# Performance work log

Measured on AMD Instinct MI355X. Metric: run time of the kernel, lower is better.

## Reference

```python
import jax, jax.numpy as jnp
import numpy as np

N, E, G = 100000, 1600000, 1000
F_IN, H, C = 16, 64, 2
EPS = 1e-5


def setup_inputs() -> dict:
    key = jax.random.key(0)
    ks = jax.random.split(key, 8)

    def lin(k, i, o):
        return (jax.random.normal(k, (i, o), jnp.float32) / np.float32(np.sqrt(i)))

    return {
        "x": jax.random.normal(ks[0], (N, F_IN), jnp.float32),
        "edge_index": jax.random.randint(ks[1], (2, E), 0, N),
        "batch": jnp.sort(jax.random.randint(ks[2], (N,), 0, G)),
        # GraphNorm params: weight=1, bias=0, mean_scale(alpha)=1 (PyG init)
        "gn0_w": jnp.ones(F_IN, jnp.float32), "gn0_b": jnp.zeros(F_IN, jnp.float32), "gn0_a": jnp.ones(F_IN, jnp.float32),
        "W1": lin(ks[3], F_IN, H), "b1": jnp.zeros(H, jnp.float32),
        "gn1_w": jnp.ones(H, jnp.float32), "gn1_b": jnp.zeros(H, jnp.float32), "gn1_a": jnp.ones(H, jnp.float32),
        "W2": lin(ks[4], H, H), "b2": jnp.zeros(H, jnp.float32),
        "gn2_w": jnp.ones(H, jnp.float32), "gn2_b": jnp.zeros(H, jnp.float32), "gn2_a": jnp.ones(H, jnp.float32),
        "W3": lin(ks[5], H, H), "b3": jnp.zeros(H, jnp.float32),
        "Wd": lin(ks[6], H, H), "bd": jnp.zeros(H, jnp.float32),
        "Wo": lin(ks[7], H, C), "bo": jnp.zeros(C, jnp.float32),
    }


def _graph_norm(x, batch, w, b, a):
    counts = jnp.maximum(jax.ops.segment_sum(jnp.ones(x.shape[0], x.dtype), batch, G), 1.0)[:, None]
    mean = jax.ops.segment_sum(x, batch, G) / counts          # [G, F]
    out = x - a * mean[batch]
    var = jax.ops.segment_sum(out * out, batch, G) / counts   # [G, F]
    return w * (out * jax.lax.rsqrt(var + EPS)[batch]) + b


def _gcn_conv(x, W, b, src, dst):
    # PyG GCNConv: D^{-1/2}(A+I)D^{-1/2} X W + b, deg includes self-loop
    h = x @ W                                                  # [N, out]
    deg = jax.ops.segment_sum(jnp.ones(src.shape[0], x.dtype), dst, N) + 1.0
    dinv = jax.lax.rsqrt(deg)
    msg = h[src] * (dinv[src] * dinv[dst])[:, None]            # [E, out]
    agg = jax.ops.segment_sum(msg, dst, N) + h / deg[:, None]  # self-loop term: 1/deg
    return agg + b


def reference(x, edge_index, batch, gn0_w, gn0_b, gn0_a, W1, b1,
              gn1_w, gn1_b, gn1_a, W2, b2, gn2_w, gn2_b, gn2_a,
              W3, b3, Wd, bd, Wo, bo):
    src, dst = edge_index[0], edge_index[1]
    x = _graph_norm(x, batch, gn0_w, gn0_b, gn0_a)
    x = jax.nn.relu(_gcn_conv(x, W1, b1, src, dst))
    x = _graph_norm(x, batch, gn1_w, gn1_b, gn1_a)
    x = jax.nn.relu(_gcn_conv(x, W2, b2, src, dst))
    x = _graph_norm(x, batch, gn2_w, gn2_b, gn2_a)
    x = jax.nn.relu(_gcn_conv(x, W3, b3, src, dst))
    counts = jnp.maximum(jax.ops.segment_sum(jnp.ones(N, x.dtype), batch, G), 1.0)
    pooled = jax.ops.segment_sum(x, batch, G) / counts[:, None]  # global_mean_pool [G, H]
    # dropout p=0.5 is identity in eval mode
    h = jax.nn.relu(pooled @ Wd + bd)
    logits = h @ Wo + bo
    return jax.nn.softmax(logits, axis=1)
```

## Files before the change

### kernel.cpp

```cpp
#include <hip/hip_runtime.h>
#include <hip/hip_fp16.h>
#include <math.h>

#define NB_NODES 100000
#define NB_EDGES 1600000
#define NB_GRAPHS 1000
#define CAP 232
#define NBLK1 400
#define CHUNK 4000
#define NBUCK 391
#define BCAP 4608
constexpr float GN_EPS = 1e-5f;

__global__ __launch_bounds__(256) void k1_hist(const int* __restrict__ dst,
    int* __restrict__ hist, const int* __restrict__ batch, int* __restrict__ gstart) {
    __shared__ int h[NBUCK];
    int tid = threadIdx.x;
    for (int i = tid; i < NBUCK; i += 256) h[i] = 0;
    if (blockIdx.x < 4) {
        int g = blockIdx.x * 256 + tid;
        if (g <= NB_GRAPHS) {
            int lo = 0, hi = NB_NODES;
            while (lo < hi) {
                int mid = (lo + hi) >> 1;
                if (batch[mid] < g) lo = mid + 1; else hi = mid;
            }
            gstart[g] = lo;
        }
    }
    __syncthreads();
    int base = blockIdx.x * CHUNK;
    for (int i = tid; i < CHUNK; i += 256) atomicAdd(&h[dst[base + i] >> 8], 1);
    __syncthreads();
    for (int i = tid; i < NBUCK; i += 256) hist[blockIdx.x * NBUCK + i] = h[i];
}

__global__ __launch_bounds__(512) void k2a_scan(int* __restrict__ hist,
                                                int* __restrict__ total) {
    __shared__ int s[512];
    int b = blockIdx.x;
    int tid = threadIdx.x;
    int v = (tid < NBLK1) ? hist[tid * NBUCK + b] : 0;
    s[tid] = v;
    __syncthreads();
    for (int o = 1; o < 512; o <<= 1) {
        int t = (tid >= o) ? s[tid - o] : 0;
        __syncthreads();
        s[tid] += t;
        __syncthreads();
    }
    if (tid < NBLK1) hist[tid * NBUCK + b] = s[tid] - v;
    if (tid == 511) total[b] = s[511];
}

__global__ __launch_bounds__(512) void k2b_scan(const int* __restrict__ total,
                                                int* __restrict__ base) {
    __shared__ int s[512];
    int tid = threadIdx.x;
    int v = (tid < NBUCK) ? total[tid] : 0;
    s[tid] = v;
    __syncthreads();
    for (int o = 1; o < 512; o <<= 1) {
        int t = (tid >= o) ? s[tid - o] : 0;
        __syncthreads();
        s[tid] += t;
        __syncthreads();
    }
    if (tid < NBUCK) base[tid] = s[tid] - v;
    if (tid == NBUCK) base[NBUCK] = NB_EDGES;
}

__global__ __launch_bounds__(256) void k3_scatter(const int* __restrict__ ei,
    const int* __restrict__ hist, const int* __restrict__ base,
    unsigned int* __restrict__ ebuf) {
    __shared__ int cur[NBUCK];
    int tid = threadIdx.x;
    for (int i = tid; i < NBUCK; i += 256)
        cur[i] = base[i] + hist[blockIdx.x * NBUCK + i];
    __syncthreads();
    int eb = blockIdx.x * CHUNK;
    for (int i = tid; i < CHUNK; i += 256) {
        int e = eb + i;
        int sidx = ei[e];
        int d = ei[NB_EDGES + e];
        int pos = atomicAdd(&cur[d >> 8], 1);
        ebuf[pos] = (unsigned int)sidx | ((unsigned int)(d & 255) << 24);
    }
}

__global__ __launch_bounds__(256) void k4_fine(const unsigned int* __restrict__ ebuf,
    const int* __restrict__ base, int* __restrict__ csr_src, int* __restrict__ rowptr,
    float* __restrict__ dinv) {
    __shared__ unsigned int epk[BCAP];
    __shared__ int outb[BCAP];
    __shared__ int cnt[256];
    __shared__ int sbuf[256];
    __shared__ int cur2[256];
    int b = blockIdx.x;
    int tid = threadIdx.x;
    int eb = base[b], ee = base[b + 1];
    int m = ee - eb;
    if (m > BCAP) m = BCAP;
    for (int i = tid; i < m; i += 256) epk[i] = ebuf[eb + i];
    cnt[tid] = 0;
    __syncthreads();
    for (int i = tid; i < m; i += 256) atomicAdd(&cnt[epk[i] >> 24], 1);
    __syncthreads();
    int c = cnt[tid];
    sbuf[tid] = c;
    __syncthreads();
    for (int o = 1; o < 256; o <<= 1) {
        int t = (tid >= o) ? sbuf[tid - o] : 0;
        __syncthreads();
        sbuf[tid] += t;
        __syncthreads();
    }
    int off = sbuf[tid] - c;
    cur2[tid] = off;
    __syncthreads();
    for (int i = tid; i < m; i += 256) {
        unsigned int p = epk[i];
        int r = atomicAdd(&cur2[p >> 24], 1);
        outb[r] = (int)(p & 0x00FFFFFFu);
    }
    __syncthreads();
    for (int i = tid; i < m; i += 256) csr_src[eb + i] = outb[i];
    int node = b * 256 + tid;
    if (node < NB_NODES) {
        rowptr[node] = eb + off;
        dinv[node] = rsqrtf((float)(c + 1));
    }
    if (b == 0 && tid == 0) rowptr[NB_NODES] = NB_EDGES;
}

union HU {
    uint4 u;
    __half2 h[4];
};

__device__ __forceinline__ void pkacc(__half2* a, uint4 v) {
    HU x; x.u = v;
    a[0] = __hadd2(a[0], x.h[0]);
    a[1] = __hadd2(a[1], x.h[1]);
    a[2] = __hadd2(a[2], x.h[2]);
    a[3] = __hadd2(a[3], x.h[3]);
}

__device__ __forceinline__ __half2 shxor_h2(__half2 v, int m) {
    union { __half2 h; int i; } u;
    u.h = v;
    u.i = __shfl_xor(u.i, m, 64);
    return u.h;
}

__global__ __launch_bounds__(256) void aggregate_h_k(const __half* __restrict__ hs,
    const int* __restrict__ rowptr, const int* __restrict__ csr_src,
    const float* __restrict__ dinv, const float* __restrict__ bias,
    __half* __restrict__ out) {
    const uint4* hsv = (const uint4*)hs;
    int wv = blockIdx.x * 4 + (threadIdx.x >> 6);
    int lane = threadIdx.x & 63;
    int f8 = lane & 7;
    int e8 = lane >> 3;
    int n0 = __builtin_amdgcn_readfirstlane(wv * 2);
    int n1 = n0 + 1;
    int s0 = rowptr[n0], e0 = rowptr[n0 + 1], e1 = rowptr[n1 + 1];
    int s1 = e0;
    int d0 = e0 - s0, d1 = e1 - s1;
    const uint4 Z = {0u, 0u, 0u, 0u};
    int idx0 = (lane < d0) ? csr_src[s0 + lane] : -1;
    int idx1 = (lane < d1) ? csr_src[s1 + lane] : -1;
    uint4 self0 = Z, self1 = Z;
    if (e8 == 0) self0 = hsv[(size_t)n0 * 8 + f8];
    if (e8 == 1) self1 = hsv[(size_t)n1 * 8 + f8];
    uint4 g0[4], g1[4];
#pragma unroll
    for (int b = 0; b < 4; b++) {
        int u = __shfl(idx0, b * 8 + e8, 64);
        g0[b] = Z;
        if (u >= 0) g0[b] = hsv[(size_t)u * 8 + f8];
        int v = __shfl(idx1, b * 8 + e8, 64);
        g1[b] = Z;
        if (v >= 0) g1[b] = hsv[(size_t)v * 8 + f8];
    }
    __half2 acc0[4], acc1[4];
    acc0[0] = acc0[1] = acc0[2] = acc0[3] = __half2{__half(0.f), __half(0.f)};
    acc1[0] = acc1[1] = acc1[2] = acc1[3] = __half2{__half(0.f), __half(0.f)};
    pkacc(acc0, self0);
    pkacc(acc1, self1);
#pragma unroll
    for (int b = 0; b < 4; b++) { pkacc(acc0, g0[b]); pkacc(acc1, g1[b]); }
    int tb0 = (d0 + 7) >> 3, tb1 = (d1 + 7) >> 3;
    for (int b = 4; b < tb0 && b < 8; b++) {
        int u = __shfl(idx0, b * 8 + e8, 64);
        if (u >= 0) pkacc(acc0, hsv[(size_t)u * 8 + f8]);
    }
    for (int b = 4; b < tb1 && b < 8; b++) {
        int v = __shfl(idx1, b * 8 + e8, 64);
        if (v >= 0) pkacc(acc1, hsv[(size_t)v * 8 + f8]);
    }
    for (int b = 8; b < tb0; b++) {
        int j = s0 + b * 8 + e8;
        if (j < e0) { int u = csr_src[j]; pkacc(acc0, hsv[(size_t)u * 8 + f8]); }
    }
    for (int b = 8; b < tb1; b++) {
        int j = s1 + b * 8 + e8;
        if (j < e1) { int v = csr_src[j]; pkacc(acc1, hsv[(size_t)v * 8 + f8]); }
    }
#pragma unroll
    for (int c = 0; c < 4; c++) {
        __half2 t = acc0[c];
        t = __hadd2(t, shxor_h2(t, 8));
        t = __hadd2(t, shxor_h2(t, 16));
        t = __hadd2(t, shxor_h2(t, 32));
        acc0[c] = t;
        __half2 u = acc1[c];
        u = __hadd2(u, shxor_h2(u, 8));
        u = __hadd2(u, shxor_h2(u, 16));
        u = __hadd2(u, shxor_h2(u, 32));
        acc1[c] = u;
    }
    if (e8 < 2) {
        int node = (e8 == 0) ? n0 : n1;
        const __half2* acc = (e8 == 0) ? acc0 : acc1;
        float dn = dinv[node];
        const float4* b4 = (const float4*)bias;
        float4 blo = b4[f8 * 2], bhi = b4[f8 * 2 + 1];
        float2 f0 = __half22float2(acc[0]);
        float2 f1 = __half22float2(acc[1]);
        float2 f2 = __half22float2(acc[2]);
        float2 f3 = __half22float2(acc[3]);
        float r[8];
        r[0] = fmaf(f0.x, dn, blo.x); r[1] = fmaf(f0.y, dn, blo.y);
        r[2] = fmaf(f1.x, dn, blo.z); r[3] = fmaf(f1.y, dn, blo.w);
        r[4] = fmaf(f2.x, dn, bhi.x); r[5] = fmaf(f2.y, dn, bhi.y);
        r[6] = fmaf(f3.x, dn, bhi.z); r[7] = fmaf(f3.y, dn, bhi.w);
#pragma unroll
        for (int c = 0; c < 8; c++) r[c] = r[c] > 0.f ? r[c] : 0.f;
        HU o;
        o.h[0] = __floats2half2_rn(r[0], r[1]);
        o.h[1] = __floats2half2_rn(r[2], r[3]);
        o.h[2] = __floats2half2_rn(r[4], r[5]);
        o.h[3] = __floats2half2_rn(r[6], r[7]);
        ((uint4*)out)[(size_t)node * 8 + f8] = o.u;
    }
}

__global__ __launch_bounds__(512) void normlin_k(const __half* __restrict__ A,
    const int* __restrict__ gstart, const float* __restrict__ gw,
    const float* __restrict__ gb, const float* __restrict__ ga,
    const float* __restrict__ W, const float* __restrict__ dinv,
    __half* __restrict__ out) {
    __shared__ float sW[64 * 64];
    __shared__ float red[512], red2[512];
    __shared__ float sam[64], ssc[64];
    __shared__ float srow[8 * 64];
    int tid = threadIdx.x, lane = tid & 63, wid = tid >> 6;
    int g = blockIdx.x;
    int s = gstart[g], e = gstart[g + 1], cnt = e - s;
    float cntf = (float)(cnt > 1 ? cnt : 1);
    for (int i = tid; i < 64 * 64; i += 512) sW[i] = W[i];
    float sum = 0.f, sq = 0.f;
    for (int i = s + wid; i < e; i += 8) {
        float v = __half2float(A[(size_t)i * 64 + lane]);
        sum += v;
        sq = fmaf(v, v, sq);
    }
    red[tid] = sum; red2[tid] = sq;
    __syncthreads();
    for (int st = 4; st > 0; st >>= 1) {
        if (wid < st) { red[tid] += red[tid + st * 64]; red2[tid] += red2[tid + st * 64]; }
        __syncthreads();
    }
    if (tid < 64) {
        float m = red[tid] / cntf, q = red2[tid] / cntf;
        float am = ga[tid] * m;
        float var = q - 2.f * am * m + am * am;
        sam[tid] = am;
        ssc[tid] = gw[tid] * rsqrtf(var + GN_EPS);
    }
    __syncthreads();
    float am = sam[lane], sc = ssc[lane], bb = gb[lane];
    for (int i = s + wid; i < e; i += 8) {
        float nv = (__half2float(A[(size_t)i * 64 + lane]) - am) * sc + bb;
        srow[wid * 64 + lane] = nv;
        float acc = 0.f;
#pragma unroll
        for (int k = 0; k < 64; k++) acc = fmaf(srow[wid * 64 + k], sW[k * 64 + lane], acc);
        out[(size_t)i * 64 + lane] = __float2half(acc * dinv[i]);
    }
}

__device__ __forceinline__ void l0_body(float* rows, int cnt, int s,
    const float* __restrict__ x, const float* __restrict__ gw,
    const float* __restrict__ gb, const float* __restrict__ ga,
    const float* sW, const float* __restrict__ dinv, __half* __restrict__ hs_out,
    float* red, float* red2, float* sstat, float* sscale, int tid) {
    int f = tid & 15, r = tid >> 4;
    int lane = tid & 63, wid = tid >> 6;
    float cntf = (float)(cnt > 1 ? cnt : 1);
    float sum = 0.f, sq = 0.f;
    for (int i = r; i < cnt; i += 32) {
        float v = x[(size_t)(s + i) * 16 + f];
        rows[i * 16 + f] = v;
        sum += v;
        sq = fmaf(v, v, sq);
    }
    red[tid] = sum; red2[tid] = sq;
    __syncthreads();
    for (int st = 16; st > 0; st >>= 1) {
        if (r < st) { red[tid] += red[tid + st * 16]; red2[tid] += red2[tid + st * 16]; }
        __syncthreads();
    }
    if (tid < 16) {
        float m = red[tid] / cntf, q = red2[tid] / cntf;
        float am = ga[tid] * m;
        sstat[tid] = am;
        sscale[tid] = gw[tid] * rsqrtf(q - 2.f * am * m + am * am + GN_EPS);
    }
    __syncthreads();
    float am = sstat[f], sc = sscale[f], bb = gb[f];
    for (int i = r; i < cnt; i += 32) rows[i * 16 + f] = (rows[i * 16 + f] - am) * sc + bb;
    __syncthreads();
    for (int i = wid; i < cnt; i += 8) {
        float acc = 0.f;
#pragma unroll
        for (int k = 0; k < 16; k++) acc = fmaf(rows[i * 16 + k], sW[k * 64 + lane], acc);
        hs_out[(size_t)(s + i) * 64 + lane] = __float2half(acc * dinv[s + i]);
    }
}

__global__ __launch_bounds__(512) void layer0_k(const float* __restrict__ x,
    const int* __restrict__ gstart, const float* __restrict__ gw,
    const float* __restrict__ gb, const float* __restrict__ ga,
    const float* __restrict__ W, const float* __restrict__ dinv,
    __half* __restrict__ hs_out, float* __restrict__ spill16) {
    __shared__ float sRows[CAP * 16];
    __shared__ float sW[16 * 64];
    __shared__ float red[512], red2[512];
    __shared__ float sstat[16], sscale[16];
    int tid = threadIdx.x;
    int g = blockIdx.x;
    int s = gstart[g], e = gstart[g + 1], cnt = e - s;
    for (int i = tid; i < 16 * 64; i += 512) sW[i] = W[i];
    __syncthreads();
    if (cnt <= CAP)
        l0_body(sRows, cnt, s, x, gw, gb, ga, sW, dinv, hs_out, red, red2, sstat, sscale, tid);
    else
        l0_body(spill16 + (size_t)s * 16, cnt, s, x, gw, gb, ga, sW, dinv, hs_out, red, red2, sstat, sscale, tid);
}

__global__ void pool_head_k(const __half* __restrict__ x, const int* __restrict__ gstart,
                            const float* __restrict__ Wd, const float* __restrict__ bd,
                            const float* __restrict__ Wo, const float* __restrict__ bo,
                            float* __restrict__ out) {
    __shared__ float red[256];
    __shared__ float sp[64];
    __shared__ float sh[64];
    __shared__ float sl[2];
    int g = blockIdx.x;
    int s = gstart[g], e = gstart[g + 1];
    int cnt = e - s;
    float cntf = (float)(cnt > 1 ? cnt : 1);
    int tid = threadIdx.x;
    int f = tid & 63, r = tid >> 6;
    float sum = 0.f;
    for (int i = s + r; i < e; i += 4) sum += __half2float(x[(size_t)i * 64 + f]);
    red[tid] = sum;
    __syncthreads();
    for (int st = 2; st > 0; st >>= 1) {
        if (r < st) red[tid] += red[tid + st * 64];
        __syncthreads();
    }
    if (tid < 64) sp[tid] = red[tid] / cntf;
    __syncthreads();
    if (tid < 64) {
        float acc = bd[tid];
        for (int k = 0; k < 64; k++) acc = fmaf(sp[k], Wd[k * 64 + tid], acc);
        sh[tid] = acc > 0.f ? acc : 0.f;
    }
    __syncthreads();
    if (tid < 2) {
        float l = bo[tid];
        for (int k = 0; k < 64; k++) l = fmaf(sh[k], Wo[k * 2 + tid], l);
        sl[tid] = l;
    }
    __syncthreads();
    if (tid < 2) {
        float m = fmaxf(sl[0], sl[1]);
        float e0 = expf(sl[0] - m), e1 = expf(sl[1] - m);
        out[g * 2 + tid] = (tid == 0 ? e0 : e1) / (e0 + e1);
    }
}

extern "C" void kernel_launch(void* const* d_in, const int* in_sizes, int n_in,
                              void* d_out, int out_size, void* d_ws, size_t ws_size,
                              hipStream_t stream) {
    const float* x    = (const float*)d_in[0];
    const int* ei     = (const int*)d_in[1];
    const int* batch  = (const int*)d_in[2];
    const float* gn0w = (const float*)d_in[3];
    const float* gn0b = (const float*)d_in[4];
    const float* gn0a = (const float*)d_in[5];
    const float* W1   = (const float*)d_in[6];
    const float* b1   = (const float*)d_in[7];
    const float* gn1w = (const float*)d_in[8];
    const float* gn1b = (const float*)d_in[9];
    const float* gn1a = (const float*)d_in[10];
    const float* W2   = (const float*)d_in[11];
    const float* b2   = (const float*)d_in[12];
    const float* gn2w = (const float*)d_in[13];
    const float* gn2b = (const float*)d_in[14];
    const float* gn2a = (const float*)d_in[15];
    const float* W3   = (const float*)d_in[16];
    const float* b3   = (const float*)d_in[17];
    const float* Wd   = (const float*)d_in[18];
    const float* bd   = (const float*)d_in[19];
    const float* Wo   = (const float*)d_in[20];
    const float* bo   = (const float*)d_in[21];

    char* p = (char*)d_ws;
    auto alloc = [&](size_t bytes) -> void* {
        void* r = (void*)p;
        p += (bytes + 255) & ~(size_t)255;
        return r;
    };
    __half* A        = (__half*)alloc((size_t)NB_NODES * 64 * 2);
    __half* B        = (__half*)alloc((size_t)NB_NODES * 64 * 2);
    int* rowptr      = (int*)alloc((size_t)(NB_NODES + 1) * 4);
    unsigned* ebuf   = (unsigned*)alloc((size_t)NB_EDGES * 4);
    int* csr_src     = (int*)alloc((size_t)NB_EDGES * 4);
    int* hist        = (int*)alloc((size_t)NBLK1 * NBUCK * 4);
    int* total       = (int*)alloc((size_t)NBUCK * 4);
    int* basearr     = (int*)alloc((size_t)(NBUCK + 1) * 4);
    float* dinv      = (float*)alloc((size_t)NB_NODES * 4);
    int* gstart      = (int*)alloc((size_t)(NB_GRAPHS + 1) * 4);
    float* spill16   = (float*)alloc((size_t)NB_NODES * 16 * 4);

    k1_hist<<<NBLK1, 256, 0, stream>>>(ei + NB_EDGES, hist, batch, gstart);
    k2a_scan<<<NBUCK, 512, 0, stream>>>(hist, total);
    k2b_scan<<<1, 512, 0, stream>>>(total, basearr);
    k3_scatter<<<NBLK1, 256, 0, stream>>>(ei, hist, basearr, ebuf);
    k4_fine<<<NBUCK, 256, 0, stream>>>(ebuf, basearr, csr_src, rowptr, dinv);

    layer0_k<<<NB_GRAPHS, 512, 0, stream>>>(x, gstart, gn0w, gn0b, gn0a, W1, dinv, B, spill16);
    aggregate_h_k<<<12500, 256, 0, stream>>>(B, rowptr, csr_src, dinv, b1, A);
    normlin_k<<<NB_GRAPHS, 512, 0, stream>>>(A, gstart, gn1w, gn1b, gn1a, W2, dinv, B);
    aggregate_h_k<<<12500, 256, 0, stream>>>(B, rowptr, csr_src, dinv, b2, A);
    normlin_k<<<NB_GRAPHS, 512, 0, stream>>>(A, gstart, gn2w, gn2b, gn2a, W3, dinv, B);
    aggregate_h_k<<<12500, 256, 0, stream>>>(B, rowptr, csr_src, dinv, b3, A);
    pool_head_k<<<NB_GRAPHS, 256, 0, stream>>>(A, gstart, Wd, bd, Wo, bo, (float*)d_out);
}
```

Before: 321.5 us.

## Fuse CSR-build kernels into one persistent kernel with grid barriers

Merges the five CSR-construction kernels (histogram, two scans, scatter, fine sort) into a single 400-block kernel separated by software grid barriers built on atomic counters, plus a memset to reset the counters. The aim is to remove the launch gaps between several small kernels. The change relies on all 400 blocks being resident at once, since otherwise the barrier deadlocks. It also adds spin-wait overhead and a larger static shared allocation per block.

```diff
diff --git a/kernel.cpp b/kernel.cpp
--- a/kernel.cpp
+++ b/kernel.cpp
@@ -12,125 +12,152 @@
 #define BCAP 4608
 constexpr float GN_EPS = 1e-5f;
 
-__global__ __launch_bounds__(256) void k1_hist(const int* __restrict__ dst,
-    int* __restrict__ hist, const int* __restrict__ batch, int* __restrict__ gstart) {
-    __shared__ int h[NBUCK];
+__device__ __forceinline__ void gbar(int* bar, int idx, int n) {
+    __syncthreads();
+    if (threadIdx.x == 0) {
+        __threadfence();
+        atomicAdd(&bar[idx], 1);
+        while (atomicAdd(&bar[idx], 0) < n) __builtin_amdgcn_s_sleep(8);
+        __threadfence();
+    }
+    __syncthreads();
+}
+
+__global__ __launch_bounds__(256) void csr_build_k(const int* __restrict__ ei,
+    const int* __restrict__ batch, int* __restrict__ gstart, int* __restrict__ hist,
+    int* __restrict__ total, int* __restrict__ base, unsigned int* __restrict__ ebuf,
+    int* __restrict__ csr_src, int* __restrict__ rowptr, float* __restrict__ dinv,
+    int* __restrict__ bar) {
+    __shared__ int shmem[2 * BCAP + 768];
+    const int* dst = ei + NB_EDGES;
     int tid = threadIdx.x;
-    for (int i = tid; i < NBUCK; i += 256) h[i] = 0;
-    if (blockIdx.x < 4) {
-        int g = blockIdx.x * 256 + tid;
-        if (g <= NB_GRAPHS) {
-            int lo = 0, hi = NB_NODES;
-            while (lo < hi) {
-                int mid = (lo + hi) >> 1;
-                if (batch[mid] < g) lo = mid + 1; else hi = mid;
+    int blk = blockIdx.x;
+
+    {
+        int* h = shmem;
+        for (int i = tid; i < NBUCK; i += 256) h[i] = 0;
+        if (blk < 4) {
+            int g = blk * 256 + tid;
+            if (g <= NB_GRAPHS) {
+                int lo = 0, hi = NB_NODES;
+                while (lo < hi) {
+                    int mid = (lo + hi) >> 1;
+                    if (batch[mid] < g) lo = mid + 1; else hi = mid;
+                }
+                gstart[g] = lo;
             }
-            gstart[g] = lo;
-        }
-    }
-    __syncthreads();
-    int base = blockIdx.x * CHUNK;
-    for (int i = tid; i < CHUNK; i += 256) atomicAdd(&h[dst[base + i] >> 8], 1);
-    __syncthreads();
-    for (int i = tid; i < NBUCK; i += 256) hist[blockIdx.x * NBUCK + i] = h[i];
-}
-
-__global__ __launch_bounds__(512) void k2a_scan(int* __restrict__ hist,
-                                                int* __restrict__ total) {
-    __shared__ int s[512];
-    int b = blockIdx.x;
-    int tid = threadIdx.x;
-    int v = (tid < NBLK1) ? hist[tid * NBUCK + b] : 0;
-    s[tid] = v;
-    __syncthreads();
-    for (int o = 1; o < 512; o <<= 1) {
-        int t = (tid >= o) ? s[tid - o] : 0;
-        __syncthreads();
-        s[tid] += t;
-        __syncthreads();
-    }
-    if (tid < NBLK1) hist[tid * NBUCK + b] = s[tid] - v;
-    if (tid == 511) total[b] = s[511];
-}
-
-__global__ __launch_bounds__(512) void k2b_scan(const int* __restrict__ total,
-                                                int* __restrict__ base) {
-    __shared__ int s[512];
-    int tid = threadIdx.x;
-    int v = (tid < NBUCK) ? total[tid] : 0;
-    s[tid] = v;
-    __syncthreads();
-    for (int o = 1; o < 512; o <<= 1) {
-        int t = (tid >= o) ? s[tid - o] : 0;
-        __syncthreads();
-        s[tid] += t;
-        __syncthreads();
-    }
-    if (tid < NBUCK) base[tid] = s[tid] - v;
-    if (tid == NBUCK) base[NBUCK] = NB_EDGES;
-}
-
-__global__ __launch_bounds__(256) void k3_scatter(const int* __restrict__ ei,
-    const int* __restrict__ hist, const int* __restrict__ base,
-    unsigned int* __restrict__ ebuf) {
-    __shared__ int cur[NBUCK];
-    int tid = threadIdx.x;
-    for (int i = tid; i < NBUCK; i += 256)
-        cur[i] = base[i] + hist[blockIdx.x * NBUCK + i];
-    __syncthreads();
-    int eb = blockIdx.x * CHUNK;
-    for (int i = tid; i < CHUNK; i += 256) {
-        int e = eb + i;
-        int sidx = ei[e];
-        int d = ei[NB_EDGES + e];
-        int pos = atomicAdd(&cur[d >> 8], 1);
-        ebuf[pos] = (unsigned int)sidx | ((unsigned int)(d & 255) << 24);
-    }
-}
-
-__global__ __launch_bounds__(256) void k4_fine(const unsigned int* __restrict__ ebuf,
-    const int* __restrict__ base, int* __restrict__ csr_src, int* __restrict__ rowptr,
-    float* __restrict__ dinv) {
-    __shared__ unsigned int epk[BCAP];
-    __shared__ int outb[BCAP];
-    __shared__ int cnt[256];
-    __shared__ int sbuf[256];
-    __shared__ int cur2[256];
-    int b = blockIdx.x;
-    int tid = threadIdx.x;
-    int eb = base[b], ee = base[b + 1];
-    int m = ee - eb;
-    if (m > BCAP) m = BCAP;
-    for (int i = tid; i < m; i += 256) epk[i] = ebuf[eb + i];
-    cnt[tid] = 0;
-    __syncthreads();
-    for (int i = tid; i < m; i += 256) atomicAdd(&cnt[epk[i] >> 24], 1);
-    __syncthreads();
-    int c = cnt[tid];
-    sbuf[tid] = c;
-    __syncthreads();
-    for (int o = 1; o < 256; o <<= 1) {
-        int t = (tid >= o) ? sbuf[tid - o] : 0;
-        __syncthreads();
-        sbuf[tid] += t;
-        __syncthreads();
-    }
-    int off = sbuf[tid] - c;
-    cur2[tid] = off;
-    __syncthreads();
-    for (int i = tid; i < m; i += 256) {
-        unsigned int p = epk[i];
-        int r = atomicAdd(&cur2[p >> 24], 1);
-        outb[r] = (int)(p & 0x00FFFFFFu);
-    }
-    __syncthreads();
-    for (int i = tid; i < m; i += 256) csr_src[eb + i] = outb[i];
-    int node = b * 256 + tid;
-    if (node < NB_NODES) {
-        rowptr[node] = eb + off;
-        dinv[node] = rsqrtf((float)(c + 1));
-    }
-    if (b == 0 && tid == 0) rowptr[NB_NODES] = NB_EDGES;
+        }
+        __syncthreads();
+        int ebase = blk * CHUNK;
+        for (int i = tid; i < CHUNK; i += 256) atomicAdd(&h[dst[ebase + i] >> 8], 1);
+        __syncthreads();
+        for (int i = tid; i < NBUCK; i += 256) hist[blk * NBUCK + i] = h[i];
+    }
+    gbar(bar, 0, NBLK1);
+
+    if (blk < NBUCK) {
+        int* s2 = shmem;
+        int b = blk;
+        int e0 = 2 * tid, e1 = 2 * tid + 1;
+        int v0 = (e0 < NBLK1) ? hist[e0 * NBUCK + b] : 0;
+        int v1 = (e1 < NBLK1) ? hist[e1 * NBUCK + b] : 0;
+        int own = v0 + v1;
+        s2[tid] = own;
+        __syncthreads();
+        for (int o = 1; o < 256; o <<= 1) {
+            int t = (tid >= o) ? s2[tid - o] : 0;
+            __syncthreads();
+            s2[tid] += t;
+            __syncthreads();
+        }
+        int pre = s2[tid] - own;
+        if (e0 < NBLK1) hist[e0 * NBUCK + b] = pre;
+        if (e1 < NBLK1) hist[e1 * NBUCK + b] = pre + v0;
+        if (tid == 255) total[b] = s2[255];
+        __syncthreads();
+    }
+    gbar(bar, 1, NBLK1);
+
+    if (blk == 0) {
+        int* s2 = shmem;
+        int e0 = 2 * tid, e1 = 2 * tid + 1;
+        int v0 = (e0 < NBUCK) ? total[e0] : 0;
+        int v1 = (e1 < NBUCK) ? total[e1] : 0;
+        int own = v0 + v1;
+        s2[tid] = own;
+        __syncthreads();
+        for (int o = 1; o < 256; o <<= 1) {
+            int t = (tid >= o) ? s2[tid - o] : 0;
+            __syncthreads();
+            s2[tid] += t;
+            __syncthreads();
+        }
+        int pre = s2[tid] - own;
+        if (e0 < NBUCK) base[e0] = pre;
+        if (e1 < NBUCK) base[e1] = pre + v0;
+        if (tid == 0) base[NBUCK] = NB_EDGES;
+        __syncthreads();
+    }
+    gbar(bar, 2, NBLK1);
+
+    {
+        int* cur = shmem;
+        for (int i = tid; i < NBUCK; i += 256)
+            cur[i] = base[i] + hist[blk * NBUCK + i];
+        __syncthreads();
+        int eb = blk * CHUNK;
+        for (int i = tid; i < CHUNK; i += 256) {
+            int e = eb + i;
+            int sidx = ei[e];
+            int d = dst[e];
+            int pos = atomicAdd(&cur[d >> 8], 1);
+            ebuf[pos] = (unsigned int)sidx | ((unsigned int)(d & 255) << 24);
+        }
+        __syncthreads();
+    }
+    gbar(bar, 3, NBLK1);
+
+    if (blk < NBUCK) {
+        unsigned int* epk = (unsigned int*)shmem;
+        int* outb = shmem + BCAP;
+        int* cnt  = shmem + 2 * BCAP;
+        int* sbuf = shmem + 2 * BCAP + 256;
+        int* cur2 = shmem + 2 * BCAP + 512;
+        int b = blk;
+        int eb = base[b], ee = base[b + 1];
+        int m = ee - eb;
+        if (m > BCAP) m = BCAP;
+        for (int i = tid; i < m; i += 256) epk[i] = ebuf[eb + i];
+        cnt[tid] = 0;
+        __syncthreads();
+        for (int i = tid; i < m; i += 256) atomicAdd(&cnt[epk[i] >> 24], 1);
+        __syncthreads();
+        int c = cnt[tid];
+        sbuf[tid] = c;
+        __syncthreads();
+        for (int o = 1; o < 256; o <<= 1) {
+            int t = (tid >= o) ? sbuf[tid - o] : 0;
+            __syncthreads();
+            sbuf[tid] += t;
+            __syncthreads();
+        }
+        int off = sbuf[tid] - c;
+        cur2[tid] = off;
+        __syncthreads();
+        for (int i = tid; i < m; i += 256) {
+            unsigned int p = epk[i];
+            int r = atomicAdd(&cur2[p >> 24], 1);
+            outb[r] = (int)(p & 0x00FFFFFFu);
+        }
+        __syncthreads();
+        for (int i = tid; i < m; i += 256) csr_src[eb + i] = outb[i];
+        int node = b * 256 + tid;
+        if (node < NB_NODES) {
+            rowptr[node] = eb + off;
+            dinv[node] = rsqrtf((float)(c + 1));
+        }
+        if (b == 0 && tid == 0) rowptr[NB_NODES] = NB_EDGES;
+    }
 }
 
 union HU {
@@ -436,12 +463,11 @@
     float* dinv      = (float*)alloc((size_t)NB_NODES * 4);
     int* gstart      = (int*)alloc((size_t)(NB_GRAPHS + 1) * 4);
     float* spill16   = (float*)alloc((size_t)NB_NODES * 16 * 4);
-
-    k1_hist<<<NBLK1, 256, 0, stream>>>(ei + NB_EDGES, hist, batch, gstart);
-    k2a_scan<<<NBUCK, 512, 0, stream>>>(hist, total);
-    k2b_scan<<<1, 512, 0, stream>>>(total, basearr);
-    k3_scatter<<<NBLK1, 256, 0, stream>>>(ei, hist, basearr, ebuf);
-    k4_fine<<<NBUCK, 256, 0, stream>>>(ebuf, basearr, csr_src, rowptr, dinv);
+    int* bar         = (int*)alloc(4 * 4);
+
+    hipMemsetAsync(bar, 0, 4 * 4, stream);
+    csr_build_k<<<NBLK1, 256, 0, stream>>>(ei, batch, gstart, hist, total, basearr,
+                                           ebuf, csr_src, rowptr, dinv, bar);
 
     layer0_k<<<NB_GRAPHS, 512, 0, stream>>>(x, gstart, gn0w, gn0b, gn0a, W1, dinv, B, spill16);
     aggregate_h_k<<<12500, 256, 0, stream>>>(B, rowptr, csr_src, dinv, b1, A);
```

Result: slower. 483.5 us (+50.4%).

## Fold bucket-base scan into scatter kernels and aggregate four nodes per wave

Applied to the files above, without the earlier changes.

Removes the single-block k2b_scan launch. Each block of k3_scatter and k4_fine now recomputes the prefix sum over bucket totals in shared memory, and k4_fine reuses its count arena for the bucket bases. The aggregation kernel now has each wave handle four destination nodes instead of two, issuing more independent neighbor gathers per wave, and the grid is halved. This trades one launch and more memory-level parallelism for redundant per-block scans and higher register pressure in the aggregation kernel.

```diff
diff --git a/kernel.cpp b/kernel.cpp
--- a/kernel.cpp
+++ b/kernel.cpp
@@ -53,30 +53,27 @@
     if (tid == 511) total[b] = s[511];
 }
 
-__global__ __launch_bounds__(512) void k2b_scan(const int* __restrict__ total,
-                                                int* __restrict__ base) {
-    __shared__ int s[512];
-    int tid = threadIdx.x;
-    int v = (tid < NBUCK) ? total[tid] : 0;
-    s[tid] = v;
-    __syncthreads();
-    for (int o = 1; o < 512; o <<= 1) {
-        int t = (tid >= o) ? s[tid - o] : 0;
-        __syncthreads();
-        s[tid] += t;
-        __syncthreads();
-    }
-    if (tid < NBUCK) base[tid] = s[tid] - v;
-    if (tid == NBUCK) base[NBUCK] = NB_EDGES;
-}
-
 __global__ __launch_bounds__(256) void k3_scatter(const int* __restrict__ ei,
-    const int* __restrict__ hist, const int* __restrict__ base,
+    const int* __restrict__ hist, const int* __restrict__ total,
     unsigned int* __restrict__ ebuf) {
     __shared__ int cur[NBUCK];
+    __shared__ int sc[256];
     int tid = threadIdx.x;
-    for (int i = tid; i < NBUCK; i += 256)
-        cur[i] = base[i] + hist[blockIdx.x * NBUCK + i];
+    int e0 = 2 * tid, e1 = 2 * tid + 1;
+    int v0 = (e0 < NBUCK) ? total[e0] : 0;
+    int v1 = (e1 < NBUCK) ? total[e1] : 0;
+    int own = v0 + v1;
+    sc[tid] = own;
+    __syncthreads();
+    for (int o = 1; o < 256; o <<= 1) {
+        int t = (tid >= o) ? sc[tid - o] : 0;
+        __syncthreads();
+        sc[tid] += t;
+        __syncthreads();
+    }
+    int pre = sc[tid] - own;
+    if (e0 < NBUCK) cur[e0] = pre + hist[blockIdx.x * NBUCK + e0];
+    if (e1 < NBUCK) cur[e1] = pre + v0 + hist[blockIdx.x * NBUCK + e1];
     __syncthreads();
     int eb = blockIdx.x * CHUNK;
     for (int i = tid; i < CHUNK; i += 256) {
@@ -89,16 +86,36 @@
 }
 
 __global__ __launch_bounds__(256) void k4_fine(const unsigned int* __restrict__ ebuf,
-    const int* __restrict__ base, int* __restrict__ csr_src, int* __restrict__ rowptr,
+    const int* __restrict__ total, int* __restrict__ csr_src, int* __restrict__ rowptr,
     float* __restrict__ dinv) {
-    __shared__ unsigned int epk[BCAP];
-    __shared__ int outb[BCAP];
-    __shared__ int cnt[256];
-    __shared__ int sbuf[256];
-    __shared__ int cur2[256];
+    __shared__ int arena[2 * BCAP + 768];
+    unsigned int* epk = (unsigned int*)arena;
+    int* outb  = arena + BCAP;
+    int* cnt   = arena + 2 * BCAP;
+    int* sbuf  = arena + 2 * BCAP + 256;
+    int* cur2  = arena + 2 * BCAP + 512;
+    int* bases = arena + 2 * BCAP;
     int b = blockIdx.x;
     int tid = threadIdx.x;
-    int eb = base[b], ee = base[b + 1];
+    int e0 = 2 * tid, e1 = 2 * tid + 1;
+    int v0 = (e0 < NBUCK) ? total[e0] : 0;
+    int v1 = (e1 < NBUCK) ? total[e1] : 0;
+    int own = v0 + v1;
+    cur2[tid] = own;
+    __syncthreads();
+    for (int o = 1; o < 256; o <<= 1) {
+        int t = (tid >= o) ? cur2[tid - o] : 0;
+        __syncthreads();
+        cur2[tid] += t;
+        __syncthreads();
+    }
+    int pre = cur2[tid] - own;
+    if (e0 < NBUCK) bases[e0] = pre;
+    if (e1 < NBUCK) bases[e1] = pre + v0;
+    if (tid == 0) bases[NBUCK] = NB_EDGES;
+    __syncthreads();
+    int eb = bases[b], ee = bases[b + 1];
+    __syncthreads();
     int m = ee - eb;
     if (m > BCAP) m = BCAP;
     for (int i = tid; i < m; i += 256) epk[i] = ebuf[eb + i];
@@ -162,67 +179,111 @@
     int lane = threadIdx.x & 63;
     int f8 = lane & 7;
     int e8 = lane >> 3;
-    int n0 = __builtin_amdgcn_readfirstlane(wv * 2);
-    int n1 = n0 + 1;
-    int s0 = rowptr[n0], e0 = rowptr[n0 + 1], e1 = rowptr[n1 + 1];
-    int s1 = e0;
-    int d0 = e0 - s0, d1 = e1 - s1;
+    int n0 = __builtin_amdgcn_readfirstlane(wv * 4);
+    int r0 = rowptr[n0], r1 = rowptr[n0 + 1], r2 = rowptr[n0 + 2];
+    int r3 = rowptr[n0 + 3], r4 = rowptr[n0 + 4];
+    int d0 = r1 - r0, d1 = r2 - r1, d2 = r3 - r2, d3 = r4 - r3;
     const uint4 Z = {0u, 0u, 0u, 0u};
-    int idx0 = (lane < d0) ? csr_src[s0 + lane] : -1;
-    int idx1 = (lane < d1) ? csr_src[s1 + lane] : -1;
-    uint4 self0 = Z, self1 = Z;
-    if (e8 == 0) self0 = hsv[(size_t)n0 * 8 + f8];
-    if (e8 == 1) self1 = hsv[(size_t)n1 * 8 + f8];
-    uint4 g0[4], g1[4];
+    int idx0 = (lane < d0) ? csr_src[r0 + lane] : -1;
+    int idx1 = (lane < d1) ? csr_src[r1 + lane] : -1;
+    int idx2 = (lane < d2) ? csr_src[r2 + lane] : -1;
+    int idx3 = (lane < d3) ? csr_src[r3 + lane] : -1;
+    uint4 self = Z;
+    if (e8 < 4) self = hsv[(size_t)(n0 + e8) * 8 + f8];
+    uint4 gA[8];
 #pragma unroll
     for (int b = 0; b < 4; b++) {
         int u = __shfl(idx0, b * 8 + e8, 64);
-        g0[b] = Z;
-        if (u >= 0) g0[b] = hsv[(size_t)u * 8 + f8];
+        gA[b] = Z;
+        if (u >= 0) gA[b] = hsv[(size_t)u * 8 + f8];
         int v = __shfl(idx1, b * 8 + e8, 64);
-        g1[b] = Z;
-        if (v >= 0) g1[b] = hsv[(size_t)v * 8 + f8];
-    }
-    __half2 acc0[4], acc1[4];
-    acc0[0] = acc0[1] = acc0[2] = acc0[3] = __half2{__half(0.f), __half(0.f)};
-    acc1[0] = acc1[1] = acc1[2] = acc1[3] = __half2{__half(0.f), __half(0.f)};
-    pkacc(acc0, self0);
-    pkacc(acc1, self1);
-#pragma unroll
-    for (int b = 0; b < 4; b++) { pkacc(acc0, g0[b]); pkacc(acc1, g1[b]); }
+        gA[4 + b] = Z;
+        if (v >= 0) gA[4 + b] = hsv[(size_t)v * 8 + f8];
+    }
+    __half2 acc0[4], acc1[4], acc2[4], acc3[4];
+    __half2 z2{__half(0.f), __half(0.f)};
+    acc0[0] = acc0[1] = acc0[2] = acc0[3] = z2;
+    acc1[0] = acc1[1] = acc1[2] = acc1[3] = z2;
+    acc2[0] = acc2[1] = acc2[2] = acc2[3] = z2;
+    acc3[0] = acc3[1] = acc3[2] = acc3[3] = z2;
+    if (e8 == 0) pkacc(acc0, self);
+    if (e8 == 1) pkacc(acc1, self);
+    if (e8 == 2) pkacc(acc2, self);
+    if (e8 == 3) pkacc(acc3, self);
+    uint4 gB[8];
+#pragma unroll
+    for (int b = 0; b < 4; b++) {
+        int u = __shfl(idx2, b * 8 + e8, 64);
+        gB[b] = Z;
+        if (u >= 0) gB[b] = hsv[(size_t)u * 8 + f8];
+        int v = __shfl(idx3, b * 8 + e8, 64);
+        gB[4 + b] = Z;
+        if (v >= 0) gB[4 + b] = hsv[(size_t)v * 8 + f8];
+    }
+#pragma unroll
+    for (int b = 0; b < 4; b++) { pkacc(acc0, gA[b]); pkacc(acc1, gA[4 + b]); }
+#pragma unroll
+    for (int b = 0; b < 4; b++) { pkacc(acc2, gB[b]); pkacc(acc3, gB[4 + b]); }
     int tb0 = (d0 + 7) >> 3, tb1 = (d1 + 7) >> 3;
+    int tb2 = (d2 + 7) >> 3, tb3 = (d3 + 7) >> 3;
     for (int b = 4; b < tb0 && b < 8; b++) {
         int u = __shfl(idx0, b * 8 + e8, 64);
         if (u >= 0) pkacc(acc0, hsv[(size_t)u * 8 + f8]);
     }
     for (int b = 4; b < tb1 && b < 8; b++) {
-        int v = __shfl(idx1, b * 8 + e8, 64);
-        if (v >= 0) pkacc(acc1, hsv[(size_t)v * 8 + f8]);
+        int u = __shfl(idx1, b * 8 + e8, 64);
+        if (u >= 0) pkacc(acc1, hsv[(size_t)u * 8 + f8]);
+    }
+    for (int b = 4; b < tb2 && b < 8; b++) {
+        int u = __shfl(idx2, b * 8 + e8, 64);
+        if (u >= 0) pkacc(acc2, hsv[(size_t)u * 8 + f8]);
+    }
+    for (int b = 4; b < tb3 && b < 8; b++) {
+        int u = __shfl(idx3, b * 8 + e8, 64);
+        if (u >= 0) pkacc(acc3, hsv[(size_t)u * 8 + f8]);
     }
     for (int b = 8; b < tb0; b++) {
-        int j = s0 + b * 8 + e8;
-        if (j < e0) { int u = csr_src[j]; pkacc(acc0, hsv[(size_t)u * 8 + f8]); }
+        int j = r0 + b * 8 + e8;
+        if (j < r1) pkacc(acc0, hsv[(size_t)csr_src[j] * 8 + f8]);
     }
     for (int b = 8; b < tb1; b++) {
-        int j = s1 + b * 8 + e8;
-        if (j < e1) { int v = csr_src[j]; pkacc(acc1, hsv[(size_t)v * 8 + f8]); }
+        int j = r1 + b * 8 + e8;
+        if (j < r2) pkacc(acc1, hsv[(size_t)csr_src[j] * 8 + f8]);
+    }
+    for (int b = 8; b < tb2; b++) {
+        int j = r2 + b * 8 + e8;
+        if (j < r3) pkacc(acc2, hsv[(size_t)csr_src[j] * 8 + f8]);
+    }
+    for (int b = 8; b < tb3; b++) {
+        int j = r3 + b * 8 + e8;
+        if (j < r4) pkacc(acc3, hsv[(size_t)csr_src[j] * 8 + f8]);
     }
 #pragma unroll
     for (int c = 0; c < 4; c++) {
-        __half2 t = acc0[c];
-        t = __hadd2(t, shxor_h2(t, 8));
-        t = __hadd2(t, shxor_h2(t, 16));
-        t = __hadd2(t, shxor_h2(t, 32));
-        acc0[c] = t;
-        __half2 u = acc1[c];
-        u = __hadd2(u, shxor_h2(u, 8));
-        u = __hadd2(u, shxor_h2(u, 16));
-        u = __hadd2(u, shxor_h2(u, 32));
-        acc1[c] = u;
-    }
-    if (e8 < 2) {
-        int node = (e8 == 0) ? n0 : n1;
-        const __half2* acc = (e8 == 0) ? acc0 : acc1;
+        __half2 t0 = acc0[c];
+        t0 = __hadd2(t0, shxor_h2(t0, 8));
+        t0 = __hadd2(t0, shxor_h2(t0, 16));
+        t0 = __hadd2(t0, shxor_h2(t0, 32));
+        acc0[c] = t0;
+        __half2 t1 = acc1[c];
+        t1 = __hadd2(t1, shxor_h2(t1, 8));
+        t1 = __hadd2(t1, shxor_h2(t1, 16));
+        t1 = __hadd2(t1, shxor_h2(t1, 32));
+        acc1[c] = t1;
+        __half2 t2 = acc2[c];
+        t2 = __hadd2(t2, shxor_h2(t2, 8));
+        t2 = __hadd2(t2, shxor_h2(t2, 16));
+        t2 = __hadd2(t2, shxor_h2(t2, 32));
+        acc2[c] = t2;
+        __half2 t3 = acc3[c];
+        t3 = __hadd2(t3, shxor_h2(t3, 8));
+        t3 = __hadd2(t3, shxor_h2(t3, 16));
+        t3 = __hadd2(t3, shxor_h2(t3, 32));
+        acc3[c] = t3;
+    }
+    if (e8 < 4) {
+        int node = n0 + e8;
+        const __half2* acc = (e8 == 0) ? acc0 : (e8 == 1) ? acc1 : (e8 == 2) ? acc2 : acc3;
         float dn = dinv[node];
         const float4* b4 = (const float4*)bias;
         float4 blo = b4[f8 * 2], bhi = b4[f8 * 2 + 1];
@@ -432,22 +493,20 @@
     int* csr_src     = (int*)alloc((size_t)NB_EDGES * 4);
     int* hist        = (int*)alloc((size_t)NBLK1 * NBUCK * 4);
     int* total       = (int*)alloc((size_t)NBUCK * 4);
-    int* basearr     = (int*)alloc((size_t)(NBUCK + 1) * 4);
     float* dinv      = (float*)alloc((size_t)NB_NODES * 4);
     int* gstart      = (int*)alloc((size_t)(NB_GRAPHS + 1) * 4);
     float* spill16   = (float*)alloc((size_t)NB_NODES * 16 * 4);
 
     k1_hist<<<NBLK1, 256, 0, stream>>>(ei + NB_EDGES, hist, batch, gstart);
     k2a_scan<<<NBUCK, 512, 0, stream>>>(hist, total);
-    k2b_scan<<<1, 512, 0, stream>>>(total, basearr);
-    k3_scatter<<<NBLK1, 256, 0, stream>>>(ei, hist, basearr, ebuf);
-    k4_fine<<<NBUCK, 256, 0, stream>>>(ebuf, basearr, csr_src, rowptr, dinv);
+    k3_scatter<<<NBLK1, 256, 0, stream>>>(ei, hist, total, ebuf);
+    k4_fine<<<NBUCK, 256, 0, stream>>>(ebuf, total, csr_src, rowptr, dinv);
 
     layer0_k<<<NB_GRAPHS, 512, 0, stream>>>(x, gstart, gn0w, gn0b, gn0a, W1, dinv, B, spill16);
-    aggregate_h_k<<<12500, 256, 0, stream>>>(B, rowptr, csr_src, dinv, b1, A);
+    aggregate_h_k<<<6250, 256, 0, stream>>>(B, rowptr, csr_src, dinv, b1, A);
     normlin_k<<<NB_GRAPHS, 512, 0, stream>>>(A, gstart, gn1w, gn1b, gn1a, W2, dinv, B);
-    aggregate_h_k<<<12500, 256, 0, stream>>>(B, rowptr, csr_src, dinv, b2, A);
+    aggregate_h_k<<<6250, 256, 0, stream>>>(B, rowptr, csr_src, dinv, b2, A);
     normlin_k<<<NB_GRAPHS, 512, 0, stream>>>(A, gstart, gn2w, gn2b, gn2a, W3, dinv, B);
-    aggregate_h_k<<<12500, 256, 0, stream>>>(B, rowptr, csr_src, dinv, b3, A);
+    aggregate_h_k<<<6250, 256, 0, stream>>>(B, rowptr, csr_src, dinv, b3, A);
     pool_head_k<<<NB_GRAPHS, 256, 0, stream>>>(A, gstart, Wd, bd, Wo, bo, (float*)d_out);
 }
```

After: 320.9 us. Within noise of the previous version (-0.2%).
